# Performance work log

Hardware: AMD Instinct MI355X
Metric: run time of the kernel (lower is better)

The kernel has to match this reference:

```python
import jax, jax.numpy as jnp
import numpy as np

LEAK = 0.01  # torch LeakyReLU default negative_slope

def lrelu(x):
    return jnp.where(x >= 0, x, LEAK * x)

def edge_conv(x, src, dst, ea, W1, b1, W2, b2):
    # message: cat(x_i=target, x_j=source, edge_attr) -> Linear -> LeakyReLU -> Linear
    m = jnp.concatenate([x[dst], x[src], ea], axis=1)          # [E, 2F+Fe]
    h = lrelu(m @ W1 + b1) @ W2 + b2                            # [E, H]
    n = x.shape[0]
    agg = jnp.full((n, h.shape[1]), jnp.inf, h.dtype).at[dst].min(h)  # scatter-min at target
    return jnp.where(jnp.isfinite(agg), agg, jnp.zeros_like(agg))     # empty nodes -> 0


def setup_inputs() -> dict:
    key = jax.random.key(0)
    ks = jax.random.split(key, 20)
    B, N, E = 4, 20000, 640000
    NF, AD, EF, H = 2, 1, 1, 8
    inp = {
        "node_features": jax.random.randint(ks[0], (B, N, NF), 0, 10, dtype=jnp.int32),
        "actions": jax.random.normal(ks[1], (B, N), dtype=jnp.float32),
        "edge_index": jax.random.randint(ks[2], (B, 2, E), 0, N, dtype=jnp.int64),
        "edge_features": jax.random.normal(ks[3], (B, E, EF), dtype=jnp.float32),
    }
    d0 = NF + AD  # 3
    def lin(k, fin, fout):
        s = 1.0 / np.sqrt(fin)
        k1, k2 = jax.random.split(k)
        return (jax.random.uniform(k1, (fin, fout), jnp.float32, -s, s),
                jax.random.uniform(k2, (fout,), jnp.float32, -s, s))
    inp["c1_W1"], inp["c1_b1"] = lin(ks[4], 2 * d0 + EF, H)
    inp["c1_W2"], inp["c1_b2"] = lin(ks[5], H, H)
    inp["c2_W1"], inp["c2_b1"] = lin(ks[6], 2 * H + 1, H)
    inp["c2_W2"], inp["c2_b2"] = lin(ks[7], H, H)
    inp["c3_W1"], inp["c3_b1"] = lin(ks[8], 2 * H + 1, H)
    inp["c3_W2"], inp["c3_b2"] = lin(ks[9], H, H)
    inp["lin_W"], inp["lin_b"] = lin(ks[10], d0 + H, 1)
    return inp


def reference(node_features, actions, edge_index, edge_features,
              c1_W1, c1_b1, c1_W2, c1_b2,
              c2_W1, c2_b1, c2_W2, c2_b2,
              c3_W1, c3_b1, c3_W2, c3_b2,
              lin_W, lin_b):
    # x = int(node_features) concat actions  -> float
    x0 = jnp.concatenate([node_features.astype(jnp.int32).astype(jnp.float32),
                          actions[..., None]], axis=-1)  # [B,N,3]

    def per_graph(x0g, eig, eag):
        src, dst = eig[0], eig[1]  # flow source_to_target: x_j=src, x_i=dst
        h = lrelu(edge_conv(x0g, src, dst, eag, c1_W1, c1_b1, c1_W2, c1_b2))
        h = lrelu(edge_conv(h, src, dst, eag, c2_W1, c2_b1, c2_W2, c2_b2))
        h = lrelu(edge_conv(h, src, dst, eag, c3_W1, c3_b1, c3_W2, c3_b2))
        xc = jnp.concatenate([x0g, h], axis=1)  # [N, 3+8]
        return jnp.sum(xc, axis=0)              # sum-pool over nodes

    pooled = jax.vmap(per_graph)(x0, edge_index, edge_features)  # [B, 11]
    return pooled @ lin_W + lin_b  # [B, 1]
```

## Files before the change

### kernel.cpp

```cpp
#include <hip/hip_runtime.h>
#include <hip/hip_cooperative_groups.h>

#define LEAK 0.01f
#define BS 128
#define PCHUNK 4096
#define PT 512
#define CT 512
#define MAXNB 256
#define CPGMAX 256
#define BARSTRIDE 64

__device__ __forceinline__ float lrelu(float v) {
    return v >= 0.f ? v : LEAK * v;
}

__device__ __forceinline__ unsigned int fmin_encode(float x) {
    unsigned int u = __float_as_uint(x);
    return (u & 0x80000000u) ? ~u : (u | 0x80000000u);
}
__device__ __forceinline__ float fmin_decode(unsigned int k) {
    unsigned int u = (k & 0x80000000u) ? (k ^ 0x80000000u) : ~k;
    return __uint_as_float(u);
}

__device__ __forceinline__ unsigned int bf16_rne(float f) {
    unsigned int u = __float_as_uint(f);
    return (u + 0x7FFFu + ((u >> 16) & 1u)) >> 16;
}

__device__ __forceinline__ void block_add(float c, float* dst) {
    __shared__ float wsum[8];
#pragma unroll
    for (int off = 32; off > 0; off >>= 1) c += __shfl_down(c, off, 64);
    int lane = threadIdx.x & 63;
    int wave = threadIdx.x >> 6;
    if (lane == 0) wsum[wave] = c;
    __syncthreads();
    if (threadIdx.x == 0) {
        float s = 0.f;
        int nw = blockDim.x >> 6;
        for (int w = 0; w < nw; ++w) s += wsum[w];
        atomicAdd(dst, s);
    }
}

__device__ __forceinline__ void graph_barrier(int* bar, int target) {
    __syncthreads();
    if (threadIdx.x == 0) {
        __threadfence();
        __hip_atomic_fetch_add(bar, 1, __ATOMIC_RELEASE, __HIP_MEMORY_SCOPE_AGENT);
        while (__hip_atomic_load(bar, __ATOMIC_RELAXED, __HIP_MEMORY_SCOPE_AGENT) <
               target)
            __builtin_amdgcn_s_sleep(16);
        __threadfence();
    }
    __syncthreads();
}


__device__ __forceinline__ void init_body(
    const int* __restrict__ nf, const float* __restrict__ act,
    const float* __restrict__ W1, const float* __restrict__ b1,
    const float* __restrict__ lw, const float* __restrict__ lb,
    float* __restrict__ a1, unsigned short* __restrict__ a2,
    float* __restrict__ out, int N, int b, int ib) {
    int t = threadIdx.x;
    int n = ib * PT + t;
    float c = 0.f;
    if (n < N) {
        size_t i = (size_t)b * N + n;
        float x0 = (float)nf[i * 2 + 0];
        float x1 = (float)nf[i * 2 + 1];
        float x2 = act[i];
        float v1[8], v2[8];
#pragma unroll
        for (int j = 0; j < 8; ++j) {
            v1[j] = b1[j] + x0 * W1[0 * 8 + j] + x1 * W1[1 * 8 + j] + x2 * W1[2 * 8 + j];
            v2[j] =         x0 * W1[3 * 8 + j] + x1 * W1[4 * 8 + j] + x2 * W1[5 * 8 + j];
        }
        float4* o1 = (float4*)(a1 + i * 8);
        o1[0] = make_float4(v1[0], v1[1], v1[2], v1[3]);
        o1[1] = make_float4(v1[4], v1[5], v1[6], v1[7]);
        unsigned int w[4];
#pragma unroll
        for (int q = 0; q < 4; ++q)
            w[q] = bf16_rne(v2[2 * q]) | (bf16_rne(v2[2 * q + 1]) << 16);
        *(int4*)(a2 + i * 8) = make_int4(w[0], w[1], w[2], w[3]);
        c = x0 * lw[0] + x1 * lw[1] + x2 * lw[2];
        if (n == 0) c += lb[0];
    }
    block_add(c, &out[b]);
}

__device__ __forceinline__ void count_body(
    const int* __restrict__ ei, int* __restrict__ cnt,
    int E, int NB, int CPG, int b, int c, int* __restrict__ lc) {
    int t = threadIdx.x;
    for (int i = t; i < NB; i += PT) lc[i] = 0;
    __syncthreads();
    int e0 = c * PCHUNK, end = min(e0 + PCHUNK, E);
    const int* drow = ei + (size_t)b * 2 * E + E;
    for (int e = e0 + t; e < end; e += PT)
        atomicAdd(&lc[drow[e] >> 7], 1);
    __syncthreads();
    int* crow = cnt + ((size_t)b * CPG + c) * NB;
    for (int i = t; i < NB; i += PT) crow[i] = lc[i];
}

__device__ __forceinline__ void scatter_body(
    const int* __restrict__ ei, const float* __restrict__ ea,
    const int* __restrict__ cnt, int2* __restrict__ cpairs,
    int* __restrict__ gofs, int E, int NB, int CPG, int b, int c,
    int* __restrict__ lc, int* __restrict__ lofs, int* __restrict__ ts) {
    int t = threadIdx.x;
    for (int i = t; i < NB; i += PT) lc[i] = 0;
    __syncthreads();
    int e0 = c * PCHUNK, end = min(e0 + PCHUNK, E);
    const int* srow = ei + (size_t)b * 2 * E;
    const int* drow = srow + E;

    int pk[PCHUNK / PT];
#pragma unroll
    for (int j = 0; j < PCHUNK / PT; ++j) {
        int e = e0 + j * PT + t;
        int p = -1;
        if (e < end) {
            int d = drow[e];
            int bin = d >> 7;
            int r = atomicAdd(&lc[bin], 1);
            p = bin | ((d & 127) << 10) | (r << 17);
        }
        pk[j] = p;
    }

    const int* cb = cnt + (size_t)b * CPG * NB;
    int partial = 0, full = 0;
    if (t < NB) {
        for (int c2 = 0; c2 < CPG; ++c2) {
            int v = cb[(size_t)c2 * NB + t];
            full += v;
            if (c2 < c) partial += v;
        }
    }
    int v = (t < NB) ? full : 0;
    ts[t] = v;
    __syncthreads();
    int incl = v;
    for (int off = 1; off < PT; off <<= 1) {
        int add = (t >= off) ? ts[t - off] : 0;
        __syncthreads();
        incl += add;
        ts[t] = incl;
        __syncthreads();
    }
    if (t < NB) lofs[t] = (incl - v) + partial;
    if (c == 0) {
        if (t < NB) gofs[(size_t)b * (NB + 1) + t] = incl - v;
        if (t == PT - 1) gofs[(size_t)b * (NB + 1) + NB] = incl;
    }
    __syncthreads();

    int2* cp = cpairs + (size_t)b * E;
#pragma unroll
    for (int j = 0; j < PCHUNK / PT; ++j) {
        int e = e0 + j * PT + t;
        if (e < end) {
            int p = pk[j];
            int bin = p & 1023;
            int dl = (p >> 10) & 127;
            int r = p >> 17;
            cp[lofs[bin] + r] =
                make_int2(srow[e] | (dl << 16), __float_as_int(ea[(size_t)b * E + e]));
        }
    }
}

__device__ __forceinline__ void conv_edge_compute(
    const float* we, const float* bb, const float* __restrict__ W2,
    int2 p, int4 raw, const float* __restrict__ a1s,
    unsigned int* __restrict__ acc) {
    int dl = (p.x >> 16) & 127;
    float eav = __int_as_float(p.y);
    unsigned int wq[4] = {(unsigned int)raw.x, (unsigned int)raw.y,
                          (unsigned int)raw.z, (unsigned int)raw.w};
    float a2v[8];
#pragma unroll
    for (int q = 0; q < 4; ++q) {
        a2v[2 * q]     = __uint_as_float(wq[q] << 16);
        a2v[2 * q + 1] = __uint_as_float(wq[q] & 0xFFFF0000u);
    }
    float h1[8];
#pragma unroll
    for (int j = 0; j < 8; ++j) {
        h1[j] = a1s[dl * 9 + j] + a2v[j];
        h1[j] = fmaf(eav, we[j], h1[j]);
        h1[j] = lrelu(h1[j]);
    }
    float h2[8];
#pragma unroll
    for (int j = 0; j < 8; ++j) h2[j] = bb[j];
#pragma unroll
    for (int kk = 0; kk < 8; ++kk) {
        float hk = h1[kk];
#pragma unroll
        for (int j = 0; j < 8; ++j) h2[j] = fmaf(hk, W2[kk * 8 + j], h2[j]);
    }
#pragma unroll
    for (int j = 0; j < 8; ++j)
        atomicMin(&acc[dl * 9 + j], fmin_encode(h2[j]));
}

__device__ __forceinline__ void conv_edges_dense(
    const unsigned short* __restrict__ a2g, const float* we, const float* bb,
    const float* __restrict__ W2, const int2* __restrict__ cpg,
    int start, int end,
    const float* __restrict__ a1s, unsigned int* __restrict__ acc) {
    int t = threadIdx.x;
    int k = start + t * 4;
    for (; k + 3 < end; k += CT * 4) {
        int2 p0 = cpg[k];
        int2 p1 = cpg[k + 1];
        int2 p2 = cpg[k + 2];
        int2 p3 = cpg[k + 3];
        int4 v0 = *(const int4*)(a2g + (size_t)(p0.x & 0xFFFF) * 8);
        int4 v1 = *(const int4*)(a2g + (size_t)(p1.x & 0xFFFF) * 8);
        int4 v2 = *(const int4*)(a2g + (size_t)(p2.x & 0xFFFF) * 8);
        int4 v3 = *(const int4*)(a2g + (size_t)(p3.x & 0xFFFF) * 8);
        conv_edge_compute(we, bb, W2, p0, v0, a1s, acc);
        conv_edge_compute(we, bb, W2, p1, v1, a1s, acc);
        conv_edge_compute(we, bb, W2, p2, v2, a1s, acc);
        conv_edge_compute(we, bb, W2, p3, v3, a1s, acc);
    }
    for (int e = k; e < end && e < k + 4; ++e) {
        int2 p = cpg[e];
        int4 v = *(const int4*)(a2g + (size_t)(p.x & 0xFFFF) * 8);
        conv_edge_compute(we, bb, W2, p, v, a1s, acc);
    }
}

__device__ __forceinline__ void conv_mid_body(
    const float* __restrict__ a1, const unsigned short* __restrict__ a2,
    const float* __restrict__ w1e, const float* __restrict__ W2,
    const float* __restrict__ b2,
    const float* __restrict__ nW1, const float* __restrict__ nb1,
    const int* __restrict__ gofs, const int2* __restrict__ cpairs,
    float* __restrict__ na1, unsigned short* __restrict__ na2,
    int N, int NB, int E, int b, int bin,
    float* __restrict__ a1s, unsigned int* __restrict__ acc) {
    int n0 = bin << 7;
    int nCnt = min(BS, N - n0);
    int t = threadIdx.x;
    size_t node0 = (size_t)b * N + n0;

    for (int i = t; i < nCnt * 8; i += CT)
        a1s[(i >> 3) * 9 + (i & 7)] = a1[node0 * 8 + i];
    for (int i = t; i < BS * 9; i += CT) acc[i] = 0xFFFFFFFFu;
    float we[8], bb[8];
#pragma unroll
    for (int j = 0; j < 8; ++j) { we[j] = w1e[j]; bb[j] = b2[j]; }
    const int* gofsb = gofs + (size_t)b * (NB + 1);
    int start = gofsb[bin];
    int end = gofsb[bin + 1];
    __syncthreads();

    conv_edges_dense(a2 + (size_t)b * N * 8, we, bb, W2,
                     cpairs + (size_t)b * E, start, end, a1s, acc);
    __syncthreads();

    for (int i = t; i < nCnt * 8; i += CT) {
        float v = fmin_decode(acc[(i >> 3) * 9 + (i & 7)]);
        unsigned int u = __float_as_uint(v);
        if ((u & 0x7F800000u) == 0x7F800000u) v = 0.f;
        a1s[(i >> 3) * 9 + (i & 7)] = lrelu(v);
    }
    __syncthreads();

    for (int nh = t; nh < nCnt * 2; nh += CT) {
        int node = nh >> 1, half = nh & 1;
        float h[8];
#pragma unroll
        for (int j = 0; j < 8; ++j) h[j] = a1s[node * 9 + j];
        float v[8];
#pragma unroll
        for (int j = 0; j < 8; ++j) v[j] = half ? 0.f : nb1[j];
        const float* Wbase = nW1 + (half ? 64 : 0);
#pragma unroll
        for (int k = 0; k < 8; ++k) {
            float hk = h[k];
#pragma unroll
            for (int j = 0; j < 8; ++j) v[j] = fmaf(hk, Wbase[k * 8 + j], v[j]);
        }
        if (half) {
            unsigned int w[4];
#pragma unroll
            for (int q = 0; q < 4; ++q)
                w[q] = bf16_rne(v[2 * q]) | (bf16_rne(v[2 * q + 1]) << 16);
            *(int4*)(na2 + (node0 + node) * 8) = make_int4(w[0], w[1], w[2], w[3]);
        } else {
            float4* o = (float4*)(na1 + (node0 + node) * 8);
            o[0] = make_float4(v[0], v[1], v[2], v[3]);
            o[1] = make_float4(v[4], v[5], v[6], v[7]);
        }
    }
    __syncthreads();
}

__device__ __forceinline__ void conv_final_body(
    const float* __restrict__ a1, const unsigned short* __restrict__ a2,
    const float* __restrict__ w1e, const float* __restrict__ W2,
    const float* __restrict__ b2, const float* __restrict__ lw,
    const int* __restrict__ gofs, const int2* __restrict__ cpairs,
    float* __restrict__ out, int N, int NB, int E, int b, int bin,
    float* __restrict__ a1s, unsigned int* __restrict__ acc) {
    int n0 = bin << 7;
    int nCnt = min(BS, N - n0);
    int t = threadIdx.x;
    size_t node0 = (size_t)b * N + n0;

    for (int i = t; i < nCnt * 8; i += CT)
        a1s[(i >> 3) * 9 + (i & 7)] = a1[node0 * 8 + i];
    for (int i = t; i < BS * 9; i += CT) acc[i] = 0xFFFFFFFFu;
    float we[8], bb[8];
#pragma unroll
    for (int j = 0; j < 8; ++j) { we[j] = w1e[j]; bb[j] = b2[j]; }
    const int* gofsb = gofs + (size_t)b * (NB + 1);
    int start = gofsb[bin];
    int end = gofsb[bin + 1];
    __syncthreads();

    conv_edges_dense(a2 + (size_t)b * N * 8, we, bb, W2,
                     cpairs + (size_t)b * E, start, end, a1s, acc);
    __syncthreads();

    float c = 0.f;
    if (t < nCnt) {
#pragma unroll
        for (int j = 0; j < 8; ++j) {
            float v = fmin_decode(acc[t * 9 + j]);
            unsigned int u = __float_as_uint(v);
            if ((u & 0x7F800000u) == 0x7F800000u) v = 0.f;
            c = fmaf(lrelu(v), lw[3 + j], c);
        }
    }
    __syncthreads();
    block_add(c, &out[b]);
}


struct MegaParams {
    const int* ei; const float* ea;
    int* cnt; int2* cpairs; int* gofs;
    const int* nf; const float* act;
    const float* W11; const float* b11; const float* W21; const float* b21;
    const float* W12; const float* b12; const float* W22; const float* b22;
    const float* W13; const float* b13; const float* W23; const float* b23;
    const float* lw; const float* lb;
    float* a1A; unsigned short* a2A; float* a1B; unsigned short* a2B;
    float* out;
    int* bar;
    int E, N, NB, CPG, initBlocks;
};

__global__ __launch_bounds__(512, 8) void mega_kernel(MegaParams P) {
    __shared__ int lc[MAXNB];
    __shared__ int lofs[MAXNB + 1];
    __shared__ int ts[PT];
    __shared__ float a1s[BS * 9];
    __shared__ unsigned int acc[BS * 9];
    int b = blockIdx.y, bx = blockIdx.x;
    int* bar = P.bar + b * BARSTRIDE;
    const int gx = gridDim.x;

    if (bx < P.CPG)
        count_body(P.ei, P.cnt, P.E, P.NB, P.CPG, b, bx, lc);
    else if (bx - P.CPG < P.initBlocks)
        init_body(P.nf, P.act, P.W11, P.b11, P.lw, P.lb, P.a1A, P.a2A, P.out,
                  P.N, b, bx - P.CPG);
    graph_barrier(bar, gx);
    if (bx < P.CPG)
        scatter_body(P.ei, P.ea, P.cnt, P.cpairs, P.gofs, P.E, P.NB, P.CPG,
                     b, bx, lc, lofs, ts);
    graph_barrier(bar, gx * 2);
    if (bx < P.NB)
        conv_mid_body(P.a1A, P.a2A, P.W11 + 6 * 8, P.W21, P.b21, P.W12, P.b12,
                      P.gofs, P.cpairs, P.a1B, P.a2B, P.N, P.NB, P.E,
                      b, bx, a1s, acc);
    graph_barrier(bar, gx * 3);
    if (bx < P.NB)
        conv_mid_body(P.a1B, P.a2B, P.W12 + 16 * 8, P.W22, P.b22, P.W13, P.b13,
                      P.gofs, P.cpairs, P.a1A, P.a2A, P.N, P.NB, P.E,
                      b, bx, a1s, acc);
    graph_barrier(bar, gx * 4);
    if (bx < P.NB)
        conv_final_body(P.a1A, P.a2A, P.W13 + 16 * 8, P.W23, P.b23, P.lw,
                        P.gofs, P.cpairs, P.out, P.N, P.NB, P.E,
                        b, bx, a1s, acc);
}


__global__ __launch_bounds__(PT) void count_init_kernel(
    const int* __restrict__ ei, int* __restrict__ cnt,
    const int* __restrict__ nf, const float* __restrict__ act,
    const float* __restrict__ W1, const float* __restrict__ b1,
    const float* __restrict__ lw, const float* __restrict__ lb,
    float* __restrict__ a1, unsigned short* __restrict__ a2,
    float* __restrict__ out, int E, int N, int NB, int CPG) {
    __shared__ int lc[MAXNB];
    int b = blockIdx.y;
    if (blockIdx.x >= CPG) {
        init_body(nf, act, W1, b1, lw, lb, a1, a2, out, N, b, blockIdx.x - CPG);
        return;
    }
    count_body(ei, cnt, E, NB, CPG, b, blockIdx.x, lc);
}

__global__ __launch_bounds__(PT) void scatter_kernel(
    const int* __restrict__ ei, const float* __restrict__ ea,
    const int* __restrict__ cnt, int2* __restrict__ cpairs,
    int* __restrict__ gofs, int E, int NB, int CPG) {
    __shared__ int lc[MAXNB];
    __shared__ int lofs[MAXNB + 1];
    __shared__ int ts[PT];
    scatter_body(ei, ea, cnt, cpairs, gofs, E, NB, CPG,
                 blockIdx.y, blockIdx.x, lc, lofs, ts);
}

__global__ __launch_bounds__(CT) void conv_mid_kernel(
    const float* __restrict__ a1, const unsigned short* __restrict__ a2,
    const float* __restrict__ w1e, const float* __restrict__ W2,
    const float* __restrict__ b2,
    const float* __restrict__ nW1, const float* __restrict__ nb1,
    const int* __restrict__ gofs, const int2* __restrict__ cpairs,
    float* __restrict__ na1, unsigned short* __restrict__ na2,
    int N, int NB, int E) {
    __shared__ float a1s[BS * 9];
    __shared__ unsigned int acc[BS * 9];
    conv_mid_body(a1, a2, w1e, W2, b2, nW1, nb1, gofs, cpairs, na1, na2,
                  N, NB, E, blockIdx.y, blockIdx.x, a1s, acc);
}

__global__ __launch_bounds__(CT) void conv_final_kernel(
    const float* __restrict__ a1, const unsigned short* __restrict__ a2,
    const float* __restrict__ w1e, const float* __restrict__ W2,
    const float* __restrict__ b2, const float* __restrict__ lw,
    const int* __restrict__ gofs, const int2* __restrict__ cpairs,
    float* __restrict__ out, int N, int NB, int E) {
    __shared__ float a1s[BS * 9];
    __shared__ unsigned int acc[BS * 9];
    conv_final_body(a1, a2, w1e, W2, b2, lw, gofs, cpairs, out,
                    N, NB, E, blockIdx.y, blockIdx.x, a1s, acc);
}


__global__ __launch_bounds__(256) void node_init_kernel(
    const int* __restrict__ nf, const float* __restrict__ act,
    float* __restrict__ x0, int BN) {
    int tid = blockIdx.x * blockDim.x + threadIdx.x;
    if (tid >= BN) return;
    x0[tid * 3 + 0] = (float)nf[tid * 2 + 0];
    x0[tid * 3 + 1] = (float)nf[tid * 2 + 1];
    x0[tid * 3 + 2] = act[tid];
}

template <int D>
__global__ __launch_bounds__(256) void edge_conv_kernel(
    const float* __restrict__ x, const int* __restrict__ ei,
    const float* __restrict__ ea,
    const float* __restrict__ W1, const float* __restrict__ b1,
    const float* __restrict__ W2, const float* __restrict__ b2,
    unsigned int* __restrict__ agg, int E, int N, int B) {
    int tid = blockIdx.x * blockDim.x + threadIdx.x;
    if (tid >= B * E) return;
    int b = tid / E;
    int e = tid - b * E;
    const int* eb = ei + (size_t)b * 2 * E;
    int s = eb[e];
    int d = eb[E + e];
    const float* xi = x + ((size_t)b * N + d) * D;
    const float* xj = x + ((size_t)b * N + s) * D;
    constexpr int M = 2 * D + 1;
    float m[M];
#pragma unroll
    for (int k = 0; k < D; ++k) { m[k] = xi[k]; m[D + k] = xj[k]; }
    m[2 * D] = ea[(size_t)b * E + e];
    float h1[8];
#pragma unroll
    for (int j = 0; j < 8; ++j) h1[j] = b1[j];
#pragma unroll
    for (int k = 0; k < M; ++k) {
        float mk = m[k];
#pragma unroll
        for (int j = 0; j < 8; ++j) h1[j] = fmaf(mk, W1[k * 8 + j], h1[j]);
    }
#pragma unroll
    for (int j = 0; j < 8; ++j) h1[j] = lrelu(h1[j]);
    float h2[8];
#pragma unroll
    for (int j = 0; j < 8; ++j) h2[j] = b2[j];
#pragma unroll
    for (int k = 0; k < 8; ++k) {
        float hk = h1[k];
#pragma unroll
        for (int j = 0; j < 8; ++j) h2[j] = fmaf(hk, W2[k * 8 + j], h2[j]);
    }
    unsigned int* ag = agg + ((size_t)b * N + d) * 8;
#pragma unroll
    for (int j = 0; j < 8; ++j) atomicMin(&ag[j], fmin_encode(h2[j]));
}

__global__ __launch_bounds__(256) void finalize_kernel(
    unsigned int* __restrict__ agg, int total) {
    int tid = blockIdx.x * blockDim.x + threadIdx.x;
    if (tid >= total) return;
    float v = fmin_decode(agg[tid]);
    unsigned int u = __float_as_uint(v);
    if ((u & 0x7F800000u) == 0x7F800000u) v = 0.f;
    ((float*)agg)[tid] = lrelu(v);
}

__global__ __launch_bounds__(256) void pool_kernel(
    const float* __restrict__ x0, const float* __restrict__ h,
    const float* __restrict__ lw, const float* __restrict__ lb,
    float* __restrict__ out, int N) {
    int b = blockIdx.y;
    int n = blockIdx.x * blockDim.x + threadIdx.x;
    float c = 0.f;
    if (n < N) {
        const float* x = x0 + ((size_t)b * N + n) * 3;
        const float* hh = h + ((size_t)b * N + n) * 8;
        c = x[0] * lw[0] + x[1] * lw[1] + x[2] * lw[2];
#pragma unroll
        for (int k = 0; k < 8; ++k) c = fmaf(hh[k], lw[3 + k], c);
        if (n == 0) c += lb[0];
    }
    block_add(c, &out[b]);
}


static inline size_t align256(size_t x) { return (x + 255) & ~(size_t)255; }

extern "C" void kernel_launch(void* const* d_in, const int* in_sizes, int n_in,
                              void* d_out, int out_size, void* d_ws, size_t ws_size,
                              hipStream_t stream) {
    const int B = 4;
    const int N = in_sizes[1] / B;
    const int E = in_sizes[2] / (2 * B);

    const int*   nf  = (const int*)d_in[0];
    const float* act = (const float*)d_in[1];
    const int*   ei  = (const int*)d_in[2];
    const float* ea  = (const float*)d_in[3];
    const float* c1_W1 = (const float*)d_in[4];
    const float* c1_b1 = (const float*)d_in[5];
    const float* c1_W2 = (const float*)d_in[6];
    const float* c1_b2 = (const float*)d_in[7];
    const float* c2_W1 = (const float*)d_in[8];
    const float* c2_b1 = (const float*)d_in[9];
    const float* c2_W2 = (const float*)d_in[10];
    const float* c2_b2 = (const float*)d_in[11];
    const float* c3_W1 = (const float*)d_in[12];
    const float* c3_b1 = (const float*)d_in[13];
    const float* c3_W2 = (const float*)d_in[14];
    const float* c3_b2 = (const float*)d_in[15];
    const float* lw    = (const float*)d_in[16];
    const float* lb    = (const float*)d_in[17];
    float* out = (float*)d_out;

    const int BN = B * N;
    const int BE = B * E;
    const int NB = (N + BS - 1) / BS;
    const int CPG = (E + PCHUNK - 1) / PCHUNK;
    const int initBlocks = (N + PT - 1) / PT;

    char* ws = (char*)d_ws;
    size_t off = 0;
    float* a1A = (float*)(ws + off);           off += align256((size_t)BN * 8 * 4);
    float* a1B = (float*)(ws + off);           off += align256((size_t)BN * 8 * 4);
    unsigned short* a2A = (unsigned short*)(ws + off); off += align256((size_t)BN * 8 * 2);
    unsigned short* a2B = (unsigned short*)(ws + off); off += align256((size_t)BN * 8 * 2);
    int* cnt    = (int*)(ws + off);    off += align256((size_t)B * CPG * NB * 4);
    int2* cpairs = (int2*)(ws + off);  off += align256((size_t)BE * 8);
    int* gofs   = (int*)(ws + off);    off += align256((size_t)B * (NB + 1) * 4);
    float* x0   = (float*)(ws + off);  off += align256((size_t)BN * 3 * 4);
    int* bar    = (int*)(ws + off);    off += align256((size_t)B * BARSTRIDE * 4);
    const bool useFast = (off <= ws_size) && (NB <= MAXNB) && (CPG <= CPGMAX) &&
                         (N <= 32768);

    hipMemsetAsync(out, 0, (size_t)B * sizeof(float), stream);

    if (useFast) {
        const int gx = (CPG + initBlocks > NB) ? (CPG + initBlocks) : NB;

        int dev = 0;
        hipGetDevice(&dev);
        int numCU = 0;
        hipDeviceGetAttribute(&numCU, hipDeviceAttributeMultiprocessorCount, dev);
        int occ = 0;
        hipOccupancyMaxActiveBlocksPerMultiprocessor(&occ, mega_kernel, 512, 0);
        const bool canCoop = (occ > 0) && ((size_t)occ * (size_t)numCU >=
                                           (size_t)gx * (size_t)B);

        if (canCoop) {
            hipMemsetAsync(bar, 0, (size_t)B * BARSTRIDE * sizeof(int), stream);
            MegaParams P;
            P.ei = ei; P.ea = ea; P.cnt = cnt; P.cpairs = cpairs; P.gofs = gofs;
            P.nf = nf; P.act = act;
            P.W11 = c1_W1; P.b11 = c1_b1; P.W21 = c1_W2; P.b21 = c1_b2;
            P.W12 = c2_W1; P.b12 = c2_b1; P.W22 = c2_W2; P.b22 = c2_b2;
            P.W13 = c3_W1; P.b13 = c3_b1; P.W23 = c3_W2; P.b23 = c3_b2;
            P.lw = lw; P.lb = lb;
            P.a1A = a1A; P.a2A = a2A; P.a1B = a1B; P.a2B = a2B;
            P.out = out; P.bar = bar;
            P.E = E; P.N = N; P.NB = NB; P.CPG = CPG; P.initBlocks = initBlocks;
            void* args[] = {&P};
            hipLaunchCooperativeKernel((void*)mega_kernel, dim3(gx, B),
                                       dim3(512), args, 0, stream);
        } else {
            dim3 pgrid(CPG + initBlocks, B);
            dim3 sgrid(CPG, B);
            dim3 cgrid(NB, B);
            count_init_kernel<<<pgrid, PT, 0, stream>>>(
                ei, cnt, nf, act, c1_W1, c1_b1, lw, lb, a1A, a2A, out,
                E, N, NB, CPG);
            scatter_kernel<<<sgrid, PT, 0, stream>>>(
                ei, ea, cnt, cpairs, gofs, E, NB, CPG);
            conv_mid_kernel<<<cgrid, CT, 0, stream>>>(
                a1A, a2A, c1_W1 + 6 * 8, c1_W2, c1_b2, c2_W1, c2_b1,
                gofs, cpairs, a1B, a2B, N, NB, E);
            conv_mid_kernel<<<cgrid, CT, 0, stream>>>(
                a1B, a2B, c2_W1 + 16 * 8, c2_W2, c2_b2, c3_W1, c3_b1,
                gofs, cpairs, a1A, a2A, N, NB, E);
            conv_final_kernel<<<cgrid, CT, 0, stream>>>(
                a1A, a2A, c3_W1 + 16 * 8, c3_W2, c3_b2, lw,
                gofs, cpairs, out, N, NB, E);
        }
    } else {
        const int egrid = (BE + 255) / 256;
        const int aggTotal = BN * 8;
        const int agrid = (aggTotal + 255) / 256;
        const size_t aggBytes = (size_t)aggTotal * 4;
        unsigned int* uA = (unsigned int*)a1A;
        unsigned int* uB = (unsigned int*)a1B;

        node_init_kernel<<<(BN + 255) / 256, 256, 0, stream>>>(nf, act, x0, BN);

        hipMemsetAsync(uA, 0xFF, aggBytes, stream);
        edge_conv_kernel<3><<<egrid, 256, 0, stream>>>(
            x0, ei, ea, c1_W1, c1_b1, c1_W2, c1_b2, uA, E, N, B);
        finalize_kernel<<<agrid, 256, 0, stream>>>(uA, aggTotal);

        hipMemsetAsync(uB, 0xFF, aggBytes, stream);
        edge_conv_kernel<8><<<egrid, 256, 0, stream>>>(
            (const float*)uA, ei, ea, c2_W1, c2_b1, c2_W2, c2_b2, uB, E, N, B);
        finalize_kernel<<<agrid, 256, 0, stream>>>(uB, aggTotal);

        hipMemsetAsync(uA, 0xFF, aggBytes, stream);
        edge_conv_kernel<8><<<egrid, 256, 0, stream>>>(
            (const float*)uB, ei, ea, c3_W1, c3_b1, c3_W2, c3_b2, uA, E, N, B);
        finalize_kernel<<<agrid, 256, 0, stream>>>(uA, aggTotal);

        dim3 plgrid((N + 255) / 256, B);
        pool_kernel<<<plgrid, 256, 0, stream>>>(x0, (const float*)uA, lw, lb, out, N);
    }
}
```

Before: 234.0 us.

## Stage scatter output in LDS sorted by bin for coalesced global writes

The scatter phase now builds a local bin-sorted copy of its chunk's edge pairs in shared memory, then copies it to global memory in consecutive runs per bin instead of writing each edge to a random global slot. The goal is better-coalesced writes to the CSR edge array. In exchange it adds an extra local prefix scan, about 32KB of shared memory per block (unioned with the conv buffers in the mega kernel), and a packed bin field in the high bits of the source word. The grid-barrier spin sleep is also shortened.

```diff
diff --git a/kernel.cpp b/kernel.cpp
--- a/kernel.cpp
+++ b/kernel.cpp
@@ -10,6 +10,8 @@
 #define CPGMAX 256
 #define BARSTRIDE 64
 
+#define SMEM_BYTES (PCHUNK * 8 + MAXNB * 4 + (MAXNB + 1) * 4 + MAXNB * 4 + PT * 4)
+
 __device__ __forceinline__ float lrelu(float v) {
     return v >= 0.f ? v : LEAK * v;
 }
@@ -51,7 +53,7 @@
         __hip_atomic_fetch_add(bar, 1, __ATOMIC_RELEASE, __HIP_MEMORY_SCOPE_AGENT);
         while (__hip_atomic_load(bar, __ATOMIC_RELAXED, __HIP_MEMORY_SCOPE_AGENT) <
                target)
-            __builtin_amdgcn_s_sleep(16);
+            __builtin_amdgcn_s_sleep(4);
         __threadfence();
     }
     __syncthreads();
@@ -111,7 +113,8 @@
     const int* __restrict__ ei, const float* __restrict__ ea,
     const int* __restrict__ cnt, int2* __restrict__ cpairs,
     int* __restrict__ gofs, int E, int NB, int CPG, int b, int c,
-    int* __restrict__ lc, int* __restrict__ lofs, int* __restrict__ ts) {
+    int2* __restrict__ stg, int* __restrict__ lc, int* __restrict__ lstart,
+    int* __restrict__ gbase, int* __restrict__ ts) {
     int t = threadIdx.x;
     for (int i = t; i < NB; i += PT) lc[i] = 0;
     __syncthreads();
@@ -132,17 +135,9 @@
         }
         pk[j] = p;
     }
-
-    const int* cb = cnt + (size_t)b * CPG * NB;
-    int partial = 0, full = 0;
-    if (t < NB) {
-        for (int c2 = 0; c2 < CPG; ++c2) {
-            int v = cb[(size_t)c2 * NB + t];
-            full += v;
-            if (c2 < c) partial += v;
-        }
-    }
-    int v = (t < NB) ? full : 0;
+    __syncthreads();
+
+    int v = (t < NB) ? lc[t] : 0;
     ts[t] = v;
     __syncthreads();
     int incl = v;
@@ -153,14 +148,37 @@
         ts[t] = incl;
         __syncthreads();
     }
-    if (t < NB) lofs[t] = (incl - v) + partial;
+    if (t < NB) lstart[t] = incl - v;
+    if (t == PT - 1) lstart[NB] = incl;
+
+    const int* cb = cnt + (size_t)b * CPG * NB;
+    int partial = 0, full = 0;
+    if (t < NB) {
+        for (int c2 = 0; c2 < CPG; ++c2) {
+            int q = cb[(size_t)c2 * NB + t];
+            full += q;
+            if (c2 < c) partial += q;
+        }
+    }
+    __syncthreads();
+    int v2 = (t < NB) ? full : 0;
+    ts[t] = v2;
+    __syncthreads();
+    int incl2 = v2;
+    for (int off = 1; off < PT; off <<= 1) {
+        int add = (t >= off) ? ts[t - off] : 0;
+        __syncthreads();
+        incl2 += add;
+        ts[t] = incl2;
+        __syncthreads();
+    }
+    if (t < NB) gbase[t] = (incl2 - v2) + partial;
     if (c == 0) {
-        if (t < NB) gofs[(size_t)b * (NB + 1) + t] = incl - v;
-        if (t == PT - 1) gofs[(size_t)b * (NB + 1) + NB] = incl;
-    }
-    __syncthreads();
-
-    int2* cp = cpairs + (size_t)b * E;
+        if (t < NB) gofs[(size_t)b * (NB + 1) + t] = incl2 - v2;
+        if (t == PT - 1) gofs[(size_t)b * (NB + 1) + NB] = incl2;
+    }
+    __syncthreads();
+
 #pragma unroll
     for (int j = 0; j < PCHUNK / PT; ++j) {
         int e = e0 + j * PT + t;
@@ -169,9 +187,19 @@
             int bin = p & 1023;
             int dl = (p >> 10) & 127;
             int r = p >> 17;
-            cp[lofs[bin] + r] =
-                make_int2(srow[e] | (dl << 16), __float_as_int(ea[(size_t)b * E + e]));
+            stg[lstart[bin] + r] =
+                make_int2(srow[e] | (dl << 16) | (bin << 23),
+                          __float_as_int(ea[(size_t)b * E + e]));
         }
+    }
+    __syncthreads();
+
+    int total = lstart[NB];
+    int2* cp = cpairs + (size_t)b * E;
+    for (int k = t; k < total; k += PT) {
+        int2 pv = stg[k];
+        int bin = (pv.x >> 23) & 255;
+        cp[gbase[bin] + (k - lstart[bin])] = pv;
     }
 }
 
@@ -362,11 +390,15 @@
 };
 
 __global__ __launch_bounds__(512, 8) void mega_kernel(MegaParams P) {
-    __shared__ int lc[MAXNB];
-    __shared__ int lofs[MAXNB + 1];
-    __shared__ int ts[PT];
-    __shared__ float a1s[BS * 9];
-    __shared__ unsigned int acc[BS * 9];
+    __shared__ __align__(16) char smem[SMEM_BYTES];
+    int2* stg   = (int2*)smem;
+    int* lc     = (int*)(smem + PCHUNK * 8);
+    int* lstart = lc + MAXNB;
+    int* gbase  = lstart + (MAXNB + 1);
+    int* ts     = gbase + MAXNB;
+    float* a1s        = (float*)smem;
+    unsigned int* acc = (unsigned int*)(smem + BS * 9 * 4);
+
     int b = blockIdx.y, bx = blockIdx.x;
     int* bar = P.bar + b * BARSTRIDE;
     const int gx = gridDim.x;
@@ -379,7 +411,7 @@
     graph_barrier(bar, gx);
     if (bx < P.CPG)
         scatter_body(P.ei, P.ea, P.cnt, P.cpairs, P.gofs, P.E, P.NB, P.CPG,
-                     b, bx, lc, lofs, ts);
+                     b, bx, stg, lc, lstart, gbase, ts);
     graph_barrier(bar, gx * 2);
     if (bx < P.NB)
         conv_mid_body(P.a1A, P.a2A, P.W11 + 6 * 8, P.W21, P.b21, P.W12, P.b12,
@@ -418,11 +450,14 @@
     const int* __restrict__ ei, const float* __restrict__ ea,
     const int* __restrict__ cnt, int2* __restrict__ cpairs,
     int* __restrict__ gofs, int E, int NB, int CPG) {
-    __shared__ int lc[MAXNB];
-    __shared__ int lofs[MAXNB + 1];
-    __shared__ int ts[PT];
+    __shared__ __align__(16) char smem[SMEM_BYTES];
+    int2* stg   = (int2*)smem;
+    int* lc     = (int*)(smem + PCHUNK * 8);
+    int* lstart = lc + MAXNB;
+    int* gbase  = lstart + (MAXNB + 1);
+    int* ts     = gbase + MAXNB;
     scatter_body(ei, ea, cnt, cpairs, gofs, E, NB, CPG,
-                 blockIdx.y, blockIdx.x, lc, lofs, ts);
+                 blockIdx.y, blockIdx.x, stg, lc, lstart, gbase, ts);
 }
 
 __global__ __launch_bounds__(CT) void conv_mid_kernel(
```

After: 224.0 us. -4.3%, faster.

## Replace cooperative megakernel with separate launches and LDS-staged bucket scatter

Applied to the files above, without the earlier changes.

Removes the cooperative mega kernel and its grid-wide spin barriers, so the fast path always runs as a sequence of ordinary kernel launches. A new per-graph prep kernel precomputes per-chunk local bucket starts and global bases, taking the prefix-sum work out of every scatter block. The scatter kernel now sorts each chunk's edges into shared memory by destination bin, then writes them out in contiguous runs, making the global stores more coalesced. The cost is extra launches, a serial per-chunk scan in prep_kernel, 32KB of LDS per scatter block, and extra workspace for the offset tables.

```diff
diff --git a/kernel.cpp b/kernel.cpp
--- a/kernel.cpp
+++ b/kernel.cpp
@@ -1,5 +1,4 @@
 #include <hip/hip_runtime.h>
-#include <hip/hip_cooperative_groups.h>
 
 #define LEAK 0.01f
 #define BS 128
@@ -8,7 +7,6 @@
 #define CT 512
 #define MAXNB 256
 #define CPGMAX 256
-#define BARSTRIDE 64
 
 __device__ __forceinline__ float lrelu(float v) {
     return v >= 0.f ? v : LEAK * v;
@@ -42,19 +40,6 @@
         for (int w = 0; w < nw; ++w) s += wsum[w];
         atomicAdd(dst, s);
     }
-}
-
-__device__ __forceinline__ void graph_barrier(int* bar, int target) {
-    __syncthreads();
-    if (threadIdx.x == 0) {
-        __threadfence();
-        __hip_atomic_fetch_add(bar, 1, __ATOMIC_RELEASE, __HIP_MEMORY_SCOPE_AGENT);
-        while (__hip_atomic_load(bar, __ATOMIC_RELAXED, __HIP_MEMORY_SCOPE_AGENT) <
-               target)
-            __builtin_amdgcn_s_sleep(16);
-        __threadfence();
-    }
-    __syncthreads();
 }
 
 
@@ -107,41 +92,29 @@
     for (int i = t; i < NB; i += PT) crow[i] = lc[i];
 }
 
-__device__ __forceinline__ void scatter_body(
-    const int* __restrict__ ei, const float* __restrict__ ea,
-    const int* __restrict__ cnt, int2* __restrict__ cpairs,
-    int* __restrict__ gofs, int E, int NB, int CPG, int b, int c,
-    int* __restrict__ lc, int* __restrict__ lofs, int* __restrict__ ts) {
-    int t = threadIdx.x;
-    for (int i = t; i < NB; i += PT) lc[i] = 0;
-    __syncthreads();
-    int e0 = c * PCHUNK, end = min(e0 + PCHUNK, E);
-    const int* srow = ei + (size_t)b * 2 * E;
-    const int* drow = srow + E;
-
-    int pk[PCHUNK / PT];
-#pragma unroll
-    for (int j = 0; j < PCHUNK / PT; ++j) {
-        int e = e0 + j * PT + t;
-        int p = -1;
-        if (e < end) {
-            int d = drow[e];
-            int bin = d >> 7;
-            int r = atomicAdd(&lc[bin], 1);
-            p = bin | ((d & 127) << 10) | (r << 17);
-        }
-        pk[j] = p;
-    }
-
+__global__ __launch_bounds__(PT) void prep_kernel(
+    const int* __restrict__ cnt, int* __restrict__ lstart_m,
+    int* __restrict__ gbase_m, int* __restrict__ gofs, int NB, int CPG) {
+    __shared__ int ts[PT];
+    int b = blockIdx.x;
+    int t = threadIdx.x;
     const int* cb = cnt + (size_t)b * CPG * NB;
-    int partial = 0, full = 0;
-    if (t < NB) {
-        for (int c2 = 0; c2 < CPG; ++c2) {
-            int v = cb[(size_t)c2 * NB + t];
-            full += v;
-            if (c2 < c) partial += v;
-        }
-    }
+    int* lsb = lstart_m + (size_t)b * CPG * NB;
+    int* gbb = gbase_m + (size_t)b * CPG * NB;
+
+    for (int c = t; c < CPG; c += PT) {
+        int run = 0;
+        for (int bin = 0; bin < NB; ++bin) {
+            int q = cb[(size_t)c * NB + bin];
+            lsb[(size_t)c * NB + bin] = run;
+            run += q;
+        }
+    }
+
+    int full = 0;
+    if (t < NB)
+        for (int c = 0; c < CPG; ++c) full += cb[(size_t)c * NB + t];
+
     int v = (t < NB) ? full : 0;
     ts[t] = v;
     __syncthreads();
@@ -153,25 +126,59 @@
         ts[t] = incl;
         __syncthreads();
     }
-    if (t < NB) lofs[t] = (incl - v) + partial;
-    if (c == 0) {
-        if (t < NB) gofs[(size_t)b * (NB + 1) + t] = incl - v;
-        if (t == PT - 1) gofs[(size_t)b * (NB + 1) + NB] = incl;
-    }
-    __syncthreads();
-
-    int2* cp = cpairs + (size_t)b * E;
+    int excl = incl - v;
+    if (t < NB) gofs[(size_t)b * (NB + 1) + t] = excl;
+    if (t == PT - 1) gofs[(size_t)b * (NB + 1) + NB] = incl;
+
+    if (t < NB) {
+        int run = excl;
+        for (int c = 0; c < CPG; ++c) {
+            gbb[(size_t)c * NB + t] = run;
+            run += cb[(size_t)c * NB + t];
+        }
+    }
+}
+
+__device__ __forceinline__ void scatter_body(
+    const int* __restrict__ ei, const float* __restrict__ ea,
+    const int* __restrict__ lstart_m, const int* __restrict__ gbase_m,
+    int2* __restrict__ cpairs, int E, int NB, int CPG, int b, int c,
+    int2* __restrict__ stg, int* __restrict__ lc, int* __restrict__ lstart,
+    int* __restrict__ gbase) {
+    int t = threadIdx.x;
+    int e0 = c * PCHUNK, end = min(e0 + PCHUNK, E);
+    const int* srow = ei + (size_t)b * 2 * E;
+    const int* drow = srow + E;
+
+    const int* lsr = lstart_m + ((size_t)b * CPG + c) * NB;
+    const int* gbr = gbase_m + ((size_t)b * CPG + c) * NB;
+    for (int i = t; i < NB; i += PT) {
+        lstart[i] = lsr[i];
+        gbase[i] = gbr[i];
+        lc[i] = 0;
+    }
+    __syncthreads();
+
 #pragma unroll
     for (int j = 0; j < PCHUNK / PT; ++j) {
         int e = e0 + j * PT + t;
         if (e < end) {
-            int p = pk[j];
-            int bin = p & 1023;
-            int dl = (p >> 10) & 127;
-            int r = p >> 17;
-            cp[lofs[bin] + r] =
-                make_int2(srow[e] | (dl << 16), __float_as_int(ea[(size_t)b * E + e]));
-        }
+            int d = drow[e];
+            int bin = d >> 7;
+            int r = atomicAdd(&lc[bin], 1);
+            stg[lstart[bin] + r] =
+                make_int2(srow[e] | ((d & 127) << 16) | (bin << 23),
+                          __float_as_int(ea[(size_t)b * E + e]));
+        }
+    }
+    __syncthreads();
+
+    int total = end - e0;
+    int2* cp = cpairs + (size_t)b * E;
+    for (int k = t; k < total; k += PT) {
+        int2 pv = stg[k];
+        int bin = (pv.x >> 23) & 255;
+        cp[gbase[bin] + (k - lstart[bin])] = pv;
     }
 }
 
@@ -347,57 +354,6 @@
 }
 
 
-struct MegaParams {
-    const int* ei; const float* ea;
-    int* cnt; int2* cpairs; int* gofs;
-    const int* nf; const float* act;
-    const float* W11; const float* b11; const float* W21; const float* b21;
-    const float* W12; const float* b12; const float* W22; const float* b22;
-    const float* W13; const float* b13; const float* W23; const float* b23;
-    const float* lw; const float* lb;
-    float* a1A; unsigned short* a2A; float* a1B; unsigned short* a2B;
-    float* out;
-    int* bar;
-    int E, N, NB, CPG, initBlocks;
-};
-
-__global__ __launch_bounds__(512, 8) void mega_kernel(MegaParams P) {
-    __shared__ int lc[MAXNB];
-    __shared__ int lofs[MAXNB + 1];
-    __shared__ int ts[PT];
-    __shared__ float a1s[BS * 9];
-    __shared__ unsigned int acc[BS * 9];
-    int b = blockIdx.y, bx = blockIdx.x;
-    int* bar = P.bar + b * BARSTRIDE;
-    const int gx = gridDim.x;
-
-    if (bx < P.CPG)
-        count_body(P.ei, P.cnt, P.E, P.NB, P.CPG, b, bx, lc);
-    else if (bx - P.CPG < P.initBlocks)
-        init_body(P.nf, P.act, P.W11, P.b11, P.lw, P.lb, P.a1A, P.a2A, P.out,
-                  P.N, b, bx - P.CPG);
-    graph_barrier(bar, gx);
-    if (bx < P.CPG)
-        scatter_body(P.ei, P.ea, P.cnt, P.cpairs, P.gofs, P.E, P.NB, P.CPG,
-                     b, bx, lc, lofs, ts);
-    graph_barrier(bar, gx * 2);
-    if (bx < P.NB)
-        conv_mid_body(P.a1A, P.a2A, P.W11 + 6 * 8, P.W21, P.b21, P.W12, P.b12,
-                      P.gofs, P.cpairs, P.a1B, P.a2B, P.N, P.NB, P.E,
-                      b, bx, a1s, acc);
-    graph_barrier(bar, gx * 3);
-    if (bx < P.NB)
-        conv_mid_body(P.a1B, P.a2B, P.W12 + 16 * 8, P.W22, P.b22, P.W13, P.b13,
-                      P.gofs, P.cpairs, P.a1A, P.a2A, P.N, P.NB, P.E,
-                      b, bx, a1s, acc);
-    graph_barrier(bar, gx * 4);
-    if (bx < P.NB)
-        conv_final_body(P.a1A, P.a2A, P.W13 + 16 * 8, P.W23, P.b23, P.lw,
-                        P.gofs, P.cpairs, P.out, P.N, P.NB, P.E,
-                        b, bx, a1s, acc);
-}
-
-
 __global__ __launch_bounds__(PT) void count_init_kernel(
     const int* __restrict__ ei, int* __restrict__ cnt,
     const int* __restrict__ nf, const float* __restrict__ act,
@@ -416,13 +372,14 @@
 
 __global__ __launch_bounds__(PT) void scatter_kernel(
     const int* __restrict__ ei, const float* __restrict__ ea,
-    const int* __restrict__ cnt, int2* __restrict__ cpairs,
-    int* __restrict__ gofs, int E, int NB, int CPG) {
+    const int* __restrict__ lstart_m, const int* __restrict__ gbase_m,
+    int2* __restrict__ cpairs, int E, int NB, int CPG) {
+    __shared__ __align__(16) int2 stg[PCHUNK];
     __shared__ int lc[MAXNB];
-    __shared__ int lofs[MAXNB + 1];
-    __shared__ int ts[PT];
-    scatter_body(ei, ea, cnt, cpairs, gofs, E, NB, CPG,
-                 blockIdx.y, blockIdx.x, lc, lofs, ts);
+    __shared__ int lstart[MAXNB];
+    __shared__ int gbase[MAXNB];
+    scatter_body(ei, ea, lstart_m, gbase_m, cpairs, E, NB, CPG,
+                 blockIdx.y, blockIdx.x, stg, lc, lstart, gbase);
 }
 
 __global__ __launch_bounds__(CT) void conv_mid_kernel(
@@ -578,62 +535,37 @@
     float* a1B = (float*)(ws + off);           off += align256((size_t)BN * 8 * 4);
     unsigned short* a2A = (unsigned short*)(ws + off); off += align256((size_t)BN * 8 * 2);
     unsigned short* a2B = (unsigned short*)(ws + off); off += align256((size_t)BN * 8 * 2);
-    int* cnt    = (int*)(ws + off);    off += align256((size_t)B * CPG * NB * 4);
+    int* cnt      = (int*)(ws + off);  off += align256((size_t)B * CPG * NB * 4);
+    int* lstart_m = (int*)(ws + off);  off += align256((size_t)B * CPG * NB * 4);
+    int* gbase_m  = (int*)(ws + off);  off += align256((size_t)B * CPG * NB * 4);
     int2* cpairs = (int2*)(ws + off);  off += align256((size_t)BE * 8);
     int* gofs   = (int*)(ws + off);    off += align256((size_t)B * (NB + 1) * 4);
     float* x0   = (float*)(ws + off);  off += align256((size_t)BN * 3 * 4);
-    int* bar    = (int*)(ws + off);    off += align256((size_t)B * BARSTRIDE * 4);
     const bool useFast = (off <= ws_size) && (NB <= MAXNB) && (CPG <= CPGMAX) &&
                          (N <= 32768);
 
     hipMemsetAsync(out, 0, (size_t)B * sizeof(float), stream);
 
     if (useFast) {
-        const int gx = (CPG + initBlocks > NB) ? (CPG + initBlocks) : NB;
-
-        int dev = 0;
-        hipGetDevice(&dev);
-        int numCU = 0;
-        hipDeviceGetAttribute(&numCU, hipDeviceAttributeMultiprocessorCount, dev);
-        int occ = 0;
-        hipOccupancyMaxActiveBlocksPerMultiprocessor(&occ, mega_kernel, 512, 0);
-        const bool canCoop = (occ > 0) && ((size_t)occ * (size_t)numCU >=
-                                           (size_t)gx * (size_t)B);
-
-        if (canCoop) {
-            hipMemsetAsync(bar, 0, (size_t)B * BARSTRIDE * sizeof(int), stream);
-            MegaParams P;
-            P.ei = ei; P.ea = ea; P.cnt = cnt; P.cpairs = cpairs; P.gofs = gofs;
-            P.nf = nf; P.act = act;
-            P.W11 = c1_W1; P.b11 = c1_b1; P.W21 = c1_W2; P.b21 = c1_b2;
-            P.W12 = c2_W1; P.b12 = c2_b1; P.W22 = c2_W2; P.b22 = c2_b2;
-            P.W13 = c3_W1; P.b13 = c3_b1; P.W23 = c3_W2; P.b23 = c3_b2;
-            P.lw = lw; P.lb = lb;
-            P.a1A = a1A; P.a2A = a2A; P.a1B = a1B; P.a2B = a2B;
-            P.out = out; P.bar = bar;
-            P.E = E; P.N = N; P.NB = NB; P.CPG = CPG; P.initBlocks = initBlocks;
-            void* args[] = {&P};
-            hipLaunchCooperativeKernel((void*)mega_kernel, dim3(gx, B),
-                                       dim3(512), args, 0, stream);
-        } else {
-            dim3 pgrid(CPG + initBlocks, B);
-            dim3 sgrid(CPG, B);
-            dim3 cgrid(NB, B);
-            count_init_kernel<<<pgrid, PT, 0, stream>>>(
-                ei, cnt, nf, act, c1_W1, c1_b1, lw, lb, a1A, a2A, out,
-                E, N, NB, CPG);
-            scatter_kernel<<<sgrid, PT, 0, stream>>>(
-                ei, ea, cnt, cpairs, gofs, E, NB, CPG);
-            conv_mid_kernel<<<cgrid, CT, 0, stream>>>(
-                a1A, a2A, c1_W1 + 6 * 8, c1_W2, c1_b2, c2_W1, c2_b1,
-                gofs, cpairs, a1B, a2B, N, NB, E);
-            conv_mid_kernel<<<cgrid, CT, 0, stream>>>(
-                a1B, a2B, c2_W1 + 16 * 8, c2_W2, c2_b2, c3_W1, c3_b1,
-                gofs, cpairs, a1A, a2A, N, NB, E);
-            conv_final_kernel<<<cgrid, CT, 0, stream>>>(
-                a1A, a2A, c3_W1 + 16 * 8, c3_W2, c3_b2, lw,
-                gofs, cpairs, out, N, NB, E);
-        }
+        dim3 pgrid(CPG + initBlocks, B);
+        dim3 sgrid(CPG, B);
+        dim3 cgrid(NB, B);
+        count_init_kernel<<<pgrid, PT, 0, stream>>>(
+            ei, cnt, nf, act, c1_W1, c1_b1, lw, lb, a1A, a2A, out,
+            E, N, NB, CPG);
+        prep_kernel<<<B, PT, 0, stream>>>(
+            cnt, lstart_m, gbase_m, gofs, NB, CPG);
+        scatter_kernel<<<sgrid, PT, 0, stream>>>(
+            ei, ea, lstart_m, gbase_m, cpairs, E, NB, CPG);
+        conv_mid_kernel<<<cgrid, CT, 0, stream>>>(
+            a1A, a2A, c1_W1 + 6 * 8, c1_W2, c1_b2, c2_W1, c2_b1,
+            gofs, cpairs, a1B, a2B, N, NB, E);
+        conv_mid_kernel<<<cgrid, CT, 0, stream>>>(
+            a1B, a2B, c2_W1 + 16 * 8, c2_W2, c2_b2, c3_W1, c3_b1,
+            gofs, cpairs, a1A, a2A, N, NB, E);
+        conv_final_kernel<<<cgrid, CT, 0, stream>>>(
+            a1A, a2A, c3_W1 + 16 * 8, c3_W2, c3_b2, lw,
+            gofs, cpairs, out, N, NB, E);
     } else {
         const int egrid = (BE + 255) / 256;
         const int aggTotal = BN * 8;
```

After: 263.8 us. 1.13x slower.
